# Performance work log

Measured on AMD Instinct MI355X. Metric: run time of the kernel, lower is better.

## Reference

```python
import jax, jax.numpy as jnp
import numpy as np

VOCAB, D, K = 100000, 300, 5

def setup_inputs() -> dict:
    key = jax.random.key(0)
    ks = jax.random.split(key, 12)
    B, BAG, L = 64, 16, 128
    token_ids = jax.random.randint(ks[0], (B * BAG, L), 0, VOCAB)
    mention_rep = jax.random.normal(ks[1], (B, BAG, D), dtype=jnp.float32)
    s = 0.05
    emb = jax.random.normal(ks[2], (VOCAB, D), dtype=jnp.float32)
    W1 = jax.random.normal(ks[3], (D, D), dtype=jnp.float32) * s
    b1 = jnp.zeros((D,), jnp.float32)
    conv_w = jax.random.normal(ks[4], (D, D, K), dtype=jnp.float32) * s  # [out, in, k]
    conv_b = jnp.zeros((D,), jnp.float32)
    W2 = jax.random.normal(ks[5], (2 * D, D), dtype=jnp.float32) * s
    b2 = jnp.zeros((D,), jnp.float32)
    W3 = jax.random.normal(ks[6], (D, D), dtype=jnp.float32) * s
    b3 = jnp.zeros((D,), jnp.float32)
    return {"token_ids": token_ids, "mention_rep": mention_rep, "emb": emb,
            "W1": W1, "b1": b1, "conv_w": conv_w, "conv_b": conv_b,
            "W2": W2, "b2": b2, "W3": W3, "b3": b3}

def reference(token_ids, mention_rep, emb, W1, b1, conv_w, conv_b, W2, b2, W3, b3):
    # fused gather+pad: [N, L, D]
    x = emb[token_ids]
    # lin1
    x = x @ W1 + b1
    # conv1d over time, VALID, stride 1: NCH layout
    xc = jnp.transpose(x, (0, 2, 1))  # [N, D, L]
    y = jax.lax.conv_general_dilated(xc, conv_w, (1,), 'VALID',
                                     dimension_numbers=('NCH', 'OIH', 'NCH'))
    y = y + conv_b[None, :, None]
    cnn_out = jnp.max(y, axis=-1)  # [N, D]
    m = mention_rep.reshape(mention_rep.shape[0] * mention_rep.shape[1], -1)  # dropout = identity (eval)
    concat = jnp.concatenate([cnn_out, m], axis=-1)
    h = jnp.tanh(concat @ W2 + b2)
    out = h @ W3 + b3  # dropout = identity (eval)
    return out
```

## Files before the change

kernel.cpp:

```cpp
#include <hip/hip_runtime.h>


#define DD   300
#define LL   128
#define TOUT 124
#define CH   16
#define XR   20
#define NSTG 8
#define BLK  320
#define KS     19
#define SLABP  6080
#define ROWP   20
#define WS_G1_OFF  0
#define WS_CV_OFF  194560
#define WS_NEEDED  1167360

typedef __attribute__((ext_vector_type(8))) _Float16 f16x8;
typedef __attribute__((ext_vector_type(4))) _Float16 f16x4;
typedef __attribute__((ext_vector_type(4))) float f32x4;
typedef __attribute__((ext_vector_type(16))) float f32x16;
typedef unsigned int   u32;
typedef unsigned short u16;
typedef __attribute__((ext_vector_type(4))) u32 u32x4;

__device__ __forceinline__ float b2f(u16 u) {
    union { float f; u32 i; } x; x.i = ((u32)u) << 16; return x.f;
}
__device__ __forceinline__ u16 f2bu(float f) {
    union { float f; u32 i; } x; x.f = f;
    u32 r = x.i + 0x7FFFu + ((x.i >> 16) & 1u);
    return (u16)(r >> 16);
}
__device__ __forceinline__ float ld(const void* p, size_t idx, int is32) {
    return is32 ? ((const float*)p)[idx] : b2f(((const u16*)p)[idx]);
}
__device__ __forceinline__ int sniff_is32(const void* W1) {
    int cnt = 0;
    const u32* w1raw = (const u32*)W1;
    for (int i = 0; i < 64; ++i) {
        u32 e = (w1raw[i] >> 7) & 0xFFu;
        cnt += (e >= 100u && e <= 126u) ? 1 : 0;
    }
    return (cnt < 32) ? 1 : 0;
}

__device__ __forceinline__ void barrier_lgkm() {
    asm volatile("s_waitcnt lgkmcnt(0)" ::: "memory");
    __builtin_amdgcn_s_barrier();
}
__device__ __forceinline__ void barrier_only() {
    __builtin_amdgcn_s_barrier();
}

__device__ __forceinline__ void unit_decomp(int u, int& o, int& kq) {
    kq = (u >= 912) ? 3 : (u >= 608) ? 2 : (u >= 304) ? 1 : 0;
    o  = u - 304 * kq;
}
__device__ __forceinline__ void g1_load(const float* W1f, int kk, int o, int kq, float r[4]) {
    const int kbase = kk * 16 + kq * 4;
    #pragma unroll
    for (int j = 0; j < 4; ++j) {
        const int k = kbase + j;
        r[j] = (k < DD && o < DD) ? W1f[(size_t)k * DD + o] : 0.f;
    }
}
__device__ __forceinline__ void g1_write(_Float16* Ws, int o, int kq, const float r[4]) {
    f16x4 v;
    #pragma unroll
    for (int j = 0; j < 4; ++j) v[j] = (_Float16)r[j];
    *(f16x4*)&Ws[o * ROWP + (kq << 2)] = v;
}
__device__ __forceinline__ void cv_load(const float* CWf, int kk, int o, int kq, float r[20]) {
    const int kbase = kk * 16 + kq * 4;
    const bool ok = (o < DD) && (kbase < DD);
    const float4* src = (const float4*)(CWf + (size_t)o * 1500 + kk * 80 + kq * 20);
    #pragma unroll
    for (int i = 0; i < 5; ++i) {
        float4 t = ok ? src[i] : float4{0.f, 0.f, 0.f, 0.f};
        r[4*i] = t.x; r[4*i+1] = t.y; r[4*i+2] = t.z; r[4*i+3] = t.w;
    }
}
__device__ __forceinline__ void cv_write(_Float16* Ws, int o, int kq, const float r[20]) {
    #pragma unroll
    for (int s = 0; s < 5; ++s) {
        f16x4 v;
        #pragma unroll
        for (int j = 0; j < 4; ++j) v[j] = (_Float16)r[j * 5 + s];
        *(f16x4*)&Ws[s * SLABP + o * ROWP + (kq << 2)] = v;
    }
}

__global__ void CNNEncoder_36258113912977_xform(
    const void* W1, const void* conv_w, void* ws)
{
    if (!sniff_is32(W1)) return;
    const int kk = blockIdx.x, part = blockIdx.y, tid = threadIdx.x;

    if (part == 0) {
        const float* W1f = (const float*)W1;
        f16x8* dst = (f16x8*)((char*)ws + WS_G1_OFF) + (size_t)kk * 640;
        for (int g = tid; g < 640; g += 512) {
            const int kc = (g >= 320) ? 1 : 0;
            const int nn = g - kc * 320;
            f16x8 v;
            #pragma unroll
            for (int e = 0; e < 8; ++e) {
                const int k = kk * 16 + kc * 8 + e;
                v[e] = (_Float16)((k < DD && nn < DD) ? W1f[(size_t)k * DD + nn] : 0.f);
            }
            dst[g] = v;
        }
    } else {
        const int s = part - 1;
        const float* CWf = (const float*)conv_w;
        f16x8* dst = (f16x8*)((char*)ws + WS_CV_OFF) + (size_t)kk * 3200 + (size_t)s * 640;
        for (int g = tid; g < 640; g += 512) {
            const int kc = (g >= 320) ? 1 : 0;
            const int nn = g - kc * 320;
            f16x8 v;
            #pragma unroll
            for (int e = 0; e < 8; ++e) {
                const int k = kk * 16 + kc * 8 + e;
                v[e] = (_Float16)((k < DD && nn < DD)
                        ? CWf[(size_t)nn * 1500 + (size_t)k * 5 + s] : 0.f);
            }
            dst[g] = v;
        }
    }
}

__global__ __launch_bounds__(512, 2) void CNNEncoder_36258113912977_kernel(
    const int* __restrict__ tok, const void* mention, const void* emb,
    const void* W1, const void* b1, const void* conv_w, const void* conv_b,
    const void* W2, const void* b2, const void* W3, const void* b3,
    void* out, const void* ws)
{
    if (!sniff_is32(W1)) return;

    __shared__ __align__(16) _Float16 XB[132 * 320];
    __shared__ __align__(16) _Float16 Ws[25600];
    __shared__ float pmax4[4][320];
    __shared__ float cbuf[2 * DD];
    __shared__ float hbuf[DD];

    const int n = blockIdx.x, tid = threadIdx.x;
    const int w   = tid >> 6;
    const int l   = tid & 63;
    const int l31 = l & 31, lh = l >> 5;
    const int wm  = w >> 1;
    const int wn  = w & 1;
    const int nbase = wn * 160;
    const int mrow0 = wm * 32;
    const int* trow = tok + (size_t)n * LL;

    const f16x8* wsG1 = (const f16x8*)((const char*)ws + WS_G1_OFF);
    const f16x8* wsCV = (const f16x8*)((const char*)ws + WS_CV_OFF);
    f16x8* WsV = (f16x8*)Ws;
    const bool hx = (tid < 128);

    for (int i = tid; i < 132 * 160; i += 512) ((u32*)XB)[i] = 0u;
    __syncthreads();

    {
        const int r = tid >> 2, q = tid & 3;
        const float* erow = (const float*)emb + (size_t)trow[r] * DD;
        for (int c = q; c < 38; c += 4) {
            f16x8 v;
            if (c < 37) {
                const float4 f0 = *(const float4*)(erow + 8 * c);
                const float4 f1 = *(const float4*)(erow + 8 * c + 4);
                v[0]=(_Float16)f0.x; v[1]=(_Float16)f0.y;
                v[2]=(_Float16)f0.z; v[3]=(_Float16)f0.w;
                v[4]=(_Float16)f1.x; v[5]=(_Float16)f1.y;
                v[6]=(_Float16)f1.z; v[7]=(_Float16)f1.w;
            } else {
                const float4 f0 = *(const float4*)(erow + 296);
                v[0]=(_Float16)f0.x; v[1]=(_Float16)f0.y;
                v[2]=(_Float16)f0.z; v[3]=(_Float16)f0.w;
                v[4]=(_Float16)0.f; v[5]=(_Float16)0.f;
                v[6]=(_Float16)0.f; v[7]=(_Float16)0.f;
            }
            const int p = c ^ (r & 7);
            *(f16x8*)&XB[r * 320 + (p << 3)] = v;
        }
    }

    f32x16 acc[5];
    #pragma unroll
    for (int nt = 0; nt < 5; ++nt)
        #pragma unroll
        for (int j = 0; j < 16; ++j) acc[nt][j] = 0.f;

    f16x8 sa, sb;
    f16x8 cs[7];

    sa = wsG1[tid];
    if (hx) sb = wsG1[512 + tid];
    __syncthreads();

    for (int kk = 0; kk < 19; ++kk) {
        WsV[tid] = sa;
        if (hx) WsV[512 + tid] = sb;
        barrier_lgkm();
        if (kk + 1 < 19) {
            const f16x8* src = wsG1 + (size_t)(kk + 1) * 640;
            sa = src[tid];
            if (hx) sb = src[512 + tid];
        } else {
            #pragma unroll
            for (int p = 0; p < 6; ++p) cs[p] = wsCV[tid + 512 * p];
            if (hx) cs[6] = wsCV[3072 + tid];
        }
        {
            const int c = 2 * kk + lh;
            const int row = mrow0 + l31;
            const f16x8 a = *(const f16x8*)&XB[row * 320 + ((c ^ (row & 7)) << 3)];
            __builtin_amdgcn_s_setprio(1);
            #pragma unroll
            for (int nt = 0; nt < 5; ++nt) {
                const int nn = nbase + nt * 32 + l31;
                const f16x8 b = *(const f16x8*)&Ws[lh * 2560 + nn * 8];
                acc[nt] = __builtin_amdgcn_mfma_f32_32x32x16_f16(a, b, acc[nt], 0, 0, 0);
            }
            __builtin_amdgcn_s_setprio(0);
        }
        barrier_only();
    }

    {
        const float* b1f = (const float*)b1;
        #pragma unroll
        for (int nt = 0; nt < 5; ++nt) {
            const int col = nbase + nt * 32 + l31;
            const float bb = (col < DD) ? b1f[col] : 0.f;
            const int cc = col >> 3, c7 = col & 7;
            #pragma unroll
            for (int q = 0; q < 4; ++q) {
                #pragma unroll
                for (int r = 0; r < 4; ++r) {
                    const int row = mrow0 + q * 8 + 4 * lh + r;
                    XB[row * 320 + ((cc ^ (row & 7)) << 3) + c7]
                        = (_Float16)(acc[nt][4 * q + r] + bb);
                }
            }
        }
    }

    #pragma unroll
    for (int nt = 0; nt < 5; ++nt)
        #pragma unroll
        for (int j = 0; j < 16; ++j) acc[nt][j] = 0.f;

    for (int kk = 0; kk < 19; ++kk) {
        #pragma unroll
        for (int p = 0; p < 6; ++p) WsV[tid + 512 * p] = cs[p];
        if (hx) WsV[3072 + tid] = cs[6];
        barrier_lgkm();
        if (kk + 1 < 19) {
            const f16x8* src = wsCV + (size_t)(kk + 1) * 3200;
            #pragma unroll
            for (int p = 0; p < 6; ++p) cs[p] = src[tid + 512 * p];
            if (hx) cs[6] = src[3072 + tid];
        }
        #pragma unroll
        for (int s = 0; s < 5; ++s) {
            const int c = 2 * kk + lh;
            const int row = mrow0 + l31 + s;
            const f16x8 a = *(const f16x8*)&XB[row * 320 + ((c ^ (row & 7)) << 3)];
            __builtin_amdgcn_s_setprio(1);
            #pragma unroll
            for (int nt = 0; nt < 5; ++nt) {
                const int nn = nbase + nt * 32 + l31;
                const f16x8 b = *(const f16x8*)&Ws[s * 5120 + lh * 2560 + nn * 8];
                acc[nt] = __builtin_amdgcn_mfma_f32_32x32x16_f16(a, b, acc[nt], 0, 0, 0);
            }
            __builtin_amdgcn_s_setprio(0);
        }
        barrier_only();
    }

    #pragma unroll
    for (int nt = 0; nt < 5; ++nt) {
        float m = -3.0e38f;
        #pragma unroll
        for (int q = 0; q < 4; ++q) {
            if (!(wm == 3 && q == 3)) {
                #pragma unroll
                for (int r = 0; r < 4; ++r) m = fmaxf(m, acc[nt][4 * q + r]);
            } else if (lh == 0) {
                #pragma unroll
                for (int r = 0; r < 4; ++r) m = fmaxf(m, acc[nt][12 + r]);
            }
        }
        m = fmaxf(m, __shfl_xor(m, 32));
        if (lh == 0) pmax4[wm][nbase + nt * 32 + l31] = m;
    }
    __syncthreads();

    if (tid < DD) {
        float m = fmaxf(fmaxf(pmax4[0][tid], pmax4[1][tid]),
                        fmaxf(pmax4[2][tid], pmax4[3][tid]));
        cbuf[tid]      = m + ((const float*)conv_b)[tid];
        cbuf[DD + tid] = ((const float*)mention)[(size_t)n * DD + tid];
    }
    __syncthreads();

    if (tid < DD) {
        const float* W2f = (const float*)W2;
        float a0 = 0.f, a1 = 0.f, a2 = 0.f, a3 = 0.f;
        for (int c = 0; c < 2 * DD; c += 4) {
            a0 += cbuf[c]     * W2f[(size_t)c * DD + tid];
            a1 += cbuf[c + 1] * W2f[(size_t)(c + 1) * DD + tid];
            a2 += cbuf[c + 2] * W2f[(size_t)(c + 2) * DD + tid];
            a3 += cbuf[c + 3] * W2f[(size_t)(c + 3) * DD + tid];
        }
        hbuf[tid] = tanhf(((const float*)b2)[tid] + (a0 + a1) + (a2 + a3));
    }
    __syncthreads();

    if (tid < DD) {
        const float* W3f = (const float*)W3;
        float a0 = 0.f, a1 = 0.f;
        for (int c = 0; c < DD; c += 2) {
            a0 += hbuf[c]     * W3f[(size_t)c * DD + tid];
            a1 += hbuf[c + 1] * W3f[(size_t)(c + 1) * DD + tid];
        }
        ((float*)out)[(size_t)n * DD + tid] = ((const float*)b3)[tid] + a0 + a1;
    }
}

__global__ __launch_bounds__(512, 2) void CNNEncoder_36258113912977_nows(
    const int* __restrict__ tok, const void* mention, const void* emb,
    const void* W1, const void* b1, const void* conv_w, const void* conv_b,
    const void* W2, const void* b2, const void* W3, const void* b3,
    void* out)
{
    if (!sniff_is32(W1)) return;

    __shared__ __align__(16) _Float16 XB[132 * 320];
    __shared__ __align__(16) _Float16 Ws[5 * SLABP];
    __shared__ float pmax2[2][304];
    __shared__ float cbuf[2 * DD];
    __shared__ float hbuf[DD];

    const int n = blockIdx.x, tid = threadIdx.x;
    const int w   = tid >> 6;
    const int l   = tid & 63;
    const int l15 = l & 15, lg = l >> 4;
    const int wm  = w >> 2;
    const int wn  = w & 3;
    const int ntw   = (wn < 3) ? 5 : 4;
    const int nbase = wn * 80;
    const int mrow0 = wm * 64;
    const int* trow = tok + (size_t)n * LL;
    const float* W1f = (const float*)W1;
    const float* CWf = (const float*)conv_w;

    int o0, kq0, o1, kq1, o2, kq2;
    unit_decomp(tid, o0, kq0);
    unit_decomp(512 + tid, o1, kq1);
    const bool act2 = (l < 24);
    unit_decomp(1024 + w * 24 + (l < 24 ? l : 0), o2, kq2);

    for (int i = tid; i < 132 * 160; i += 512) ((u32*)XB)[i] = 0u;
    __syncthreads();

    {
        const int r = tid >> 2, q = tid & 3;
        const float* erow = (const float*)emb + (size_t)trow[r] * DD;
        for (int c = q; c < 38; c += 4) {
            f16x8 v;
            if (c < 37) {
                const float4 f0 = *(const float4*)(erow + 8 * c);
                const float4 f1 = *(const float4*)(erow + 8 * c + 4);
                v[0]=(_Float16)f0.x; v[1]=(_Float16)f0.y;
                v[2]=(_Float16)f0.z; v[3]=(_Float16)f0.w;
                v[4]=(_Float16)f1.x; v[5]=(_Float16)f1.y;
                v[6]=(_Float16)f1.z; v[7]=(_Float16)f1.w;
            } else {
                const float4 f0 = *(const float4*)(erow + 296);
                v[0]=(_Float16)f0.x; v[1]=(_Float16)f0.y;
                v[2]=(_Float16)f0.z; v[3]=(_Float16)f0.w;
                v[4]=(_Float16)0.f; v[5]=(_Float16)0.f;
                v[6]=(_Float16)0.f; v[7]=(_Float16)0.f;
            }
            const int p = c ^ (r & 7);
            *(f16x8*)&XB[r * 320 + (p << 3)] = v;
        }
    }

    f32x4 acc[4][5];
    const f32x4 vzero = {0.f, 0.f, 0.f, 0.f};
    #pragma unroll
    for (int mt = 0; mt < 4; ++mt)
        #pragma unroll
        for (int nt = 0; nt < 5; ++nt) acc[mt][nt] = vzero;

    float g1a[4], g1b[4], g1c[4];
    float cfa[20], cfb[20], cfc[20];

    g1_load(W1f, 0, o0, kq0, g1a);
    g1_load(W1f, 0, o1, kq1, g1b);
    if (act2) g1_load(W1f, 0, o2, kq2, g1c);
    __syncthreads();

    for (int kk = 0; kk < KS; ++kk) {
        g1_write(Ws, o0, kq0, g1a);
        g1_write(Ws, o1, kq1, g1b);
        if (act2) g1_write(Ws, o2, kq2, g1c);
        barrier_lgkm();
        if (kk + 1 < KS) {
            g1_load(W1f, kk + 1, o0, kq0, g1a);
            g1_load(W1f, kk + 1, o1, kq1, g1b);
            if (act2) g1_load(W1f, kk + 1, o2, kq2, g1c);
        } else {
            cv_load(CWf, 0, o0, kq0, cfa);
            cv_load(CWf, 0, o1, kq1, cfb);
            if (act2) cv_load(CWf, 0, o2, kq2, cfc);
        }
        {
            f16x4 af[4];
            #pragma unroll
            for (int mt = 0; mt < 4; ++mt) {
                const int row = mrow0 + mt * 16 + l15;
                const int c = (kk << 1) + (lg >> 1);
                af[mt] = *(const f16x4*)&XB[row * 320 + ((c ^ (row & 7)) << 3) + ((lg & 1) << 2)];
            }
            #pragma unroll
            for (int nt = 0; nt < 5; ++nt) {
                if (nt < ntw) {
                    const int nn = nbase + nt * 16 + l15;
                    const f16x4 b = *(const f16x4*)&Ws[nn * ROWP + (lg << 2)];
                    #pragma unroll
                    for (int mt = 0; mt < 4; ++mt)
                        acc[mt][nt] = __builtin_amdgcn_mfma_f32_16x16x16f16(af[mt], b, acc[mt][nt], 0, 0, 0);
                }
            }
        }
        barrier_only();
    }

    {
        const float* b1f = (const float*)b1;
        #pragma unroll
        for (int nt = 0; nt < 5; ++nt) {
            if (nt < ntw) {
                const int col = nbase + nt * 16 + l15;
                const float bb = (col < DD) ? b1f[col] : 0.f;
                #pragma unroll
                for (int mt = 0; mt < 4; ++mt) {
                    #pragma unroll
                    for (int j = 0; j < 4; ++j) {
                        const int row = mrow0 + mt * 16 + (lg << 2) + j;
                        XB[row * 320 + (((col >> 3) ^ (row & 7)) << 3) + (col & 7)]
                            = (_Float16)(acc[mt][nt][j] + bb);
                    }
                }
            }
        }
    }

    #pragma unroll
    for (int mt = 0; mt < 4; ++mt)
        #pragma unroll
        for (int nt = 0; nt < 5; ++nt) acc[mt][nt] = vzero;

    for (int kk = 0; kk < KS; ++kk) {
        cv_write(Ws, o0, kq0, cfa);
        cv_write(Ws, o1, kq1, cfb);
        if (act2) cv_write(Ws, o2, kq2, cfc);
        barrier_lgkm();
        if (kk + 1 < KS) {
            cv_load(CWf, kk + 1, o0, kq0, cfa);
            cv_load(CWf, kk + 1, o1, kq1, cfb);
            if (act2) cv_load(CWf, kk + 1, o2, kq2, cfc);
        }
        #pragma unroll
        for (int s = 0; s < 5; ++s) {
            f16x4 af[4];
            #pragma unroll
            for (int mt = 0; mt < 4; ++mt) {
                const int row = mrow0 + mt * 16 + l15 + s;
                const int c = (kk << 1) + (lg >> 1);
                af[mt] = *(const f16x4*)&XB[row * 320 + ((c ^ (row & 7)) << 3) + ((lg & 1) << 2)];
            }
            #pragma unroll
            for (int nt = 0; nt < 5; ++nt) {
                if (nt < ntw) {
                    const int nn = nbase + nt * 16 + l15;
                    const f16x4 b = *(const f16x4*)&Ws[s * SLABP + nn * ROWP + (lg << 2)];
                    #pragma unroll
                    for (int mt = 0; mt < 4; ++mt)
                        acc[mt][nt] = __builtin_amdgcn_mfma_f32_16x16x16f16(af[mt], b, acc[mt][nt], 0, 0, 0);
                }
            }
        }
        barrier_only();
    }

    #pragma unroll
    for (int nt = 0; nt < 5; ++nt) {
        if (nt < ntw) {
            float m = -3.0e38f;
            #pragma unroll
            for (int mt = 0; mt < 4; ++mt) {
                #pragma unroll
                for (int j = 0; j < 4; ++j) {
                    const int t = mrow0 + mt * 16 + (lg << 2) + j;
                    if (t < TOUT) m = fmaxf(m, acc[mt][nt][j]);
                }
            }
            m = fmaxf(m, __shfl_xor(m, 16));
            m = fmaxf(m, __shfl_xor(m, 32));
            if (lg == 0) pmax2[wm][nbase + nt * 16 + l15] = m;
        }
    }
    __syncthreads();

    if (tid < DD) {
        const float m = fmaxf(pmax2[0][tid], pmax2[1][tid]);
        cbuf[tid]      = m + ((const float*)conv_b)[tid];
        cbuf[DD + tid] = ((const float*)mention)[(size_t)n * DD + tid];
    }
    __syncthreads();

    if (tid < DD) {
        const float* W2f = (const float*)W2;
        float a0 = 0.f, a1 = 0.f, a2 = 0.f, a3 = 0.f;
        for (int c = 0; c < 2 * DD; c += 4) {
            a0 += cbuf[c]     * W2f[(size_t)c * DD + tid];
            a1 += cbuf[c + 1] * W2f[(size_t)(c + 1) * DD + tid];
            a2 += cbuf[c + 2] * W2f[(size_t)(c + 2) * DD + tid];
            a3 += cbuf[c + 3] * W2f[(size_t)(c + 3) * DD + tid];
        }
        hbuf[tid] = tanhf(((const float*)b2)[tid] + (a0 + a1) + (a2 + a3));
    }
    __syncthreads();

    if (tid < DD) {
        const float* W3f = (const float*)W3;
        float a0 = 0.f, a1 = 0.f;
        for (int c = 0; c < DD; c += 2) {
            a0 += hbuf[c]     * W3f[(size_t)c * DD + tid];
            a1 += hbuf[c + 1] * W3f[(size_t)(c + 1) * DD + tid];
        }
        ((float*)out)[(size_t)n * DD + tid] = ((const float*)b3)[tid] + a0 + a1;
    }
}

__global__ void CNNEncoder_36258113912977_fallback(
    const int* tok, const void* mention, const void* emb,
    const void* W1, const void* b1, const void* conv_w, const void* conv_b,
    const void* W2, const void* b2, const void* W3, const void* b3,
    void* out)
{
    __shared__ float g[XR * DD];
    __shared__ float xh[XR * DD];
    __shared__ float concat[2 * DD];
    __shared__ float hbuf[DD];

    const int n = blockIdx.x, tid = threadIdx.x;
    const int* trow = tok + (size_t)n * LL;

    if (sniff_is32(W1)) return;
    const int is32 = 0;

    float mmax = -3.0e38f;

    for (int stage = 0; stage < NSTG; ++stage) {
        const int tbase = stage * CH;
        __syncthreads();

        for (int i = tid; i < XR * DD; i += BLK) {
            int r = i / DD, c = i - (i / DD) * DD;
            int gr = tbase + r; if (gr > 127) gr = 127;
            g[i] = ld(emb, (size_t)trow[gr] * DD + c, is32);
        }
        __syncthreads();

        if (tid < DD) {
            float acc[XR];
            #pragma unroll
            for (int r = 0; r < XR; ++r) acc[r] = 0.f;
            for (int k = 0; k < DD; ++k) {
                float wv = ld(W1, (size_t)k * DD + tid, is32);
                #pragma unroll
                for (int r = 0; r < XR; ++r) acc[r] += g[r * DD + k] * wv;
            }
            float bb = ld(b1, tid, is32);
            #pragma unroll
            for (int r = 0; r < XR; ++r) xh[r * DD + tid] = acc[r] + bb;
        }
        __syncthreads();

        if (tid < DD) {
            float y[CH];
            #pragma unroll
            for (int t = 0; t < CH; ++t) y[t] = 0.f;
            const size_t cwoff = (size_t)tid * (DD * 5);
            for (int k = 0; k < DD; ++k) {
                #pragma unroll
                for (int s = 0; s < 5; ++s) {
                    float wv = ld(conv_w, cwoff + k * 5 + s, is32);
                    #pragma unroll
                    for (int t = 0; t < CH; ++t)
                        y[t] += xh[(t + s) * DD + k] * wv;
                }
            }
            #pragma unroll
            for (int t = 0; t < CH; ++t) {
                int tt = tbase + t;
                if (tt < TOUT) mmax = fmaxf(mmax, y[t]);
            }
        }
    }

    __syncthreads();
    if (tid < DD) {
        concat[tid]      = mmax + ld(conv_b, tid, is32);
        concat[DD + tid] = ld(mention, (size_t)n * DD + tid, is32);
    }
    __syncthreads();

    if (tid < DD) {
        float a = ld(b2, tid, is32);
        for (int c = 0; c < 2 * DD; ++c)
            a += concat[c] * ld(W2, (size_t)c * DD + tid, is32);
        hbuf[tid] = tanhf(a);
    }
    __syncthreads();

    if (tid < DD) {
        float a = ld(b3, tid, is32);
        for (int c = 0; c < DD; ++c)
            a += hbuf[c] * ld(W3, (size_t)c * DD + tid, is32);
        ((u16*)out)[(size_t)n * DD + tid] = f2bu(a);
    }
}

extern "C" void kernel_launch(void* const* d_in, const int* in_sizes, int n_in,
                              void* d_out, int out_size, void* d_ws, size_t ws_size,
                              hipStream_t stream)
{
    if (ws_size >= (size_t)WS_NEEDED && d_ws != nullptr) {
        CNNEncoder_36258113912977_xform<<<dim3(19, 6), 512, 0, stream>>>(
            d_in[3], d_in[5], d_ws);
        CNNEncoder_36258113912977_kernel<<<1024, 512, 0, stream>>>(
            (const int*)d_in[0], d_in[1], d_in[2], d_in[3], d_in[4], d_in[5],
            d_in[6], d_in[7], d_in[8], d_in[9], d_in[10], d_out, d_ws);
    } else {
        CNNEncoder_36258113912977_nows<<<1024, 512, 0, stream>>>(
            (const int*)d_in[0], d_in[1], d_in[2], d_in[3], d_in[4], d_in[5],
            d_in[6], d_in[7], d_in[8], d_in[9], d_in[10], d_out);
    }
    CNNEncoder_36258113912977_fallback<<<1024, BLK, 0, stream>>>(
        (const int*)d_in[0], d_in[1], d_in[2], d_in[3], d_in[4], d_in[5],
        d_in[6], d_in[7], d_in[8], d_in[9], d_in[10], d_out);
}
```

Measured before the change: 462.3 us.

## Stream lin1 and conv weights through a unified 6-slot LDS ring pipeline

```diff
diff --git a/kernel.cpp b/kernel.cpp
--- a/kernel.cpp
+++ b/kernel.cpp
@@ -14,6 +14,7 @@
 #define WS_G1_OFF  0
 #define WS_CV_OFF  194560
 #define WS_NEEDED  1167360
+#define NPH        114
 
 typedef __attribute__((ext_vector_type(8))) _Float16 f16x8;
 typedef __attribute__((ext_vector_type(4))) _Float16 f16x4;
@@ -46,9 +47,6 @@
 
 __device__ __forceinline__ void barrier_lgkm() {
     asm volatile("s_waitcnt lgkmcnt(0)" ::: "memory");
-    __builtin_amdgcn_s_barrier();
-}
-__device__ __forceinline__ void barrier_only() {
     __builtin_amdgcn_s_barrier();
 }
 
@@ -129,6 +127,41 @@
     }
 }
 
+#define STAGE_PH(P, Q, QX) do {                                             \
+    const int wr_ = (P) + 5;                                                \
+    if (wr_ < NPH) {                                                        \
+        _Float16* d_ = &ring[(wr_ % 6) * 5120];                             \
+        *(u32x4*)&d_[tid * 8] = Q;                                          \
+        if (tid < 128) *(u32x4*)&d_[(512 + tid) * 8] = QX;                  \
+    }                                                                       \
+    const int lp_ = (P) + 7;                                                \
+    if (lp_ < NPH) {                                                        \
+        const u32x4* s_ = (const u32x4*)wsAll + (size_t)lp_ * 640;          \
+        Q = s_[tid];                                                        \
+        if (tid < 128) QX = s_[512 + tid];                                  \
+    }                                                                       \
+} while (0)
+
+#define PH_BODY(P, SROW, KKC, Q, QX) do {                                   \
+    STAGE_PH((P), Q, QX);                                                   \
+    const int phys_ = (P) % 6;                                              \
+    const int c_ = 2 * (KKC) + lh;                                          \
+    const int row_ = mrow0 + l31 + (SROW);                                  \
+    const f16x8 a_ = *(const f16x8*)&XB[row_ * 320 + ((c_ ^ (row_ & 7)) << 3)]; \
+    __builtin_amdgcn_s_setprio(1);                                          \
+    _Pragma("unroll")                                                       \
+    for (int nt_ = 0; nt_ < 5; ++nt_) {                                     \
+        const int nn_ = nbase + nt_ * 32 + l31;                             \
+        const f16x8 b_ = *(const f16x8*)&ring[phys_ * 5120 + lh * 2560 + nn_ * 8]; \
+        acc[nt_] = __builtin_amdgcn_mfma_f32_32x32x16_f16(a_, b_, acc[nt_], 0, 0, 0); \
+    }                                                                       \
+    __builtin_amdgcn_s_setprio(0);                                          \
+    barrier_lgkm();                                                         \
+} while (0)
+
+#define PH_G1(KK, Q, QX)    PH_BODY((KK), 0, (KK), Q, QX)
+#define PH_CV(KK, S, Q, QX) PH_BODY(19 + (KK) * 5 + (S), (S), (KK), Q, QX)
+
 __global__ __launch_bounds__(512, 2) void CNNEncoder_36258113912977_kernel(
     const int* __restrict__ tok, const void* mention, const void* emb,
     const void* W1, const void* b1, const void* conv_w, const void* conv_b,
@@ -138,7 +171,7 @@
     if (!sniff_is32(W1)) return;
 
     __shared__ __align__(16) _Float16 XB[132 * 320];
-    __shared__ __align__(16) _Float16 Ws[25600];
+    __shared__ __align__(16) _Float16 ring[6 * 5120];
     __shared__ float pmax4[4][320];
     __shared__ float cbuf[2 * DD];
     __shared__ float hbuf[DD];
@@ -152,11 +185,21 @@
     const int nbase = wn * 160;
     const int mrow0 = wm * 32;
     const int* trow = tok + (size_t)n * LL;
-
-    const f16x8* wsG1 = (const f16x8*)((const char*)ws + WS_G1_OFF);
-    const f16x8* wsCV = (const f16x8*)((const char*)ws + WS_CV_OFF);
-    f16x8* WsV = (f16x8*)Ws;
-    const bool hx = (tid < 128);
+    const void* wsAll = ws;
+
+    u32x4 qE, qO, qEx, qOx;
+    u32x4 pre[5], prex[5];
+
+    #pragma unroll
+    for (int pl = 0; pl < 5; ++pl) {
+        const u32x4* s_ = (const u32x4*)wsAll + (size_t)pl * 640;
+        pre[pl] = s_[tid];
+        if (tid < 128) prex[pl] = s_[512 + tid];
+    }
+    { const u32x4* s_ = (const u32x4*)wsAll + (size_t)5 * 640;
+      qE = s_[tid]; if (tid < 128) qEx = s_[512 + tid]; }
+    { const u32x4* s_ = (const u32x4*)wsAll + (size_t)6 * 640;
+      qO = s_[tid]; if (tid < 128) qOx = s_[512 + tid]; }
 
     for (int i = tid; i < 132 * 160; i += 512) ((u32*)XB)[i] = 0u;
     __syncthreads();
@@ -185,47 +228,24 @@
         }
     }
 
+    #pragma unroll
+    for (int pl = 0; pl < 5; ++pl) {
+        *(u32x4*)&ring[pl * 5120 + tid * 8] = pre[pl];
+        if (tid < 128) *(u32x4*)&ring[pl * 5120 + (512 + tid) * 8] = prex[pl];
+    }
+    __syncthreads();
+
     f32x16 acc[5];
     #pragma unroll
     for (int nt = 0; nt < 5; ++nt)
         #pragma unroll
         for (int j = 0; j < 16; ++j) acc[nt][j] = 0.f;
 
-    f16x8 sa, sb;
-    f16x8 cs[7];
-
-    sa = wsG1[tid];
-    if (hx) sb = wsG1[512 + tid];
-    __syncthreads();
-
-    for (int kk = 0; kk < 19; ++kk) {
-        WsV[tid] = sa;
-        if (hx) WsV[512 + tid] = sb;
-        barrier_lgkm();
-        if (kk + 1 < 19) {
-            const f16x8* src = wsG1 + (size_t)(kk + 1) * 640;
-            sa = src[tid];
-            if (hx) sb = src[512 + tid];
-        } else {
-            #pragma unroll
-            for (int p = 0; p < 6; ++p) cs[p] = wsCV[tid + 512 * p];
-            if (hx) cs[6] = wsCV[3072 + tid];
-        }
-        {
-            const int c = 2 * kk + lh;
-            const int row = mrow0 + l31;
-            const f16x8 a = *(const f16x8*)&XB[row * 320 + ((c ^ (row & 7)) << 3)];
-            __builtin_amdgcn_s_setprio(1);
-            #pragma unroll
-            for (int nt = 0; nt < 5; ++nt) {
-                const int nn = nbase + nt * 32 + l31;
-                const f16x8 b = *(const f16x8*)&Ws[lh * 2560 + nn * 8];
-                acc[nt] = __builtin_amdgcn_mfma_f32_32x32x16_f16(a, b, acc[nt], 0, 0, 0);
-            }
-            __builtin_amdgcn_s_setprio(0);
-        }
-        barrier_only();
-    }
+    for (int kk = 0; kk < 18; kk += 2) {
+        PH_G1(kk,     qE, qEx);
+        PH_G1(kk + 1, qO, qOx);
+    }
+    PH_G1(18, qE, qEx);
 
     {
         const float* b1f = (const float*)b1;
@@ -245,39 +265,24 @@
             }
         }
     }
+    __syncthreads();
 
     #pragma unroll
     for (int nt = 0; nt < 5; ++nt)
         #pragma unroll
         for (int j = 0; j < 16; ++j) acc[nt][j] = 0.f;
 
-    for (int kk = 0; kk < 19; ++kk) {
-        #pragma unroll
-        for (int p = 0; p < 6; ++p) WsV[tid + 512 * p] = cs[p];
-        if (hx) WsV[3072 + tid] = cs[6];
-        barrier_lgkm();
-        if (kk + 1 < 19) {
-            const f16x8* src = wsCV + (size_t)(kk + 1) * 3200;
-            #pragma unroll
-            for (int p = 0; p < 6; ++p) cs[p] = src[tid + 512 * p];
-            if (hx) cs[6] = src[3072 + tid];
-        }
-        #pragma unroll
-        for (int s = 0; s < 5; ++s) {
-            const int c = 2 * kk + lh;
-            const int row = mrow0 + l31 + s;
-            const f16x8 a = *(const f16x8*)&XB[row * 320 + ((c ^ (row & 7)) << 3)];
-            __builtin_amdgcn_s_setprio(1);
-            #pragma unroll
-            for (int nt = 0; nt < 5; ++nt) {
-                const int nn = nbase + nt * 32 + l31;
-                const f16x8 b = *(const f16x8*)&Ws[s * 5120 + lh * 2560 + nn * 8];
-                acc[nt] = __builtin_amdgcn_mfma_f32_32x32x16_f16(a, b, acc[nt], 0, 0, 0);
-            }
-            __builtin_amdgcn_s_setprio(0);
-        }
-        barrier_only();
-    }
+    for (int kk = 0; kk < 18; kk += 2) {
+        PH_CV(kk, 0, qO, qOx);  PH_CV(kk, 1, qE, qEx);
+        PH_CV(kk, 2, qO, qOx);  PH_CV(kk, 3, qE, qEx);
+        PH_CV(kk, 4, qO, qOx);
+        PH_CV(kk + 1, 0, qE, qEx);  PH_CV(kk + 1, 1, qO, qOx);
+        PH_CV(kk + 1, 2, qE, qEx);  PH_CV(kk + 1, 3, qO, qOx);
+        PH_CV(kk + 1, 4, qE, qEx);
+    }
+    PH_CV(18, 0, qO, qOx);  PH_CV(18, 1, qE, qEx);
+    PH_CV(18, 2, qO, qOx);  PH_CV(18, 3, qE, qEx);
+    PH_CV(18, 4, qO, qOx);
 
     #pragma unroll
     for (int nt = 0; nt < 5; ++nt) {
@@ -437,7 +442,7 @@
                 }
             }
         }
-        barrier_only();
+        __builtin_amdgcn_s_barrier();
     }
 
     {
@@ -495,7 +500,7 @@
                 }
             }
         }
-        barrier_only();
+        __builtin_amdgcn_s_barrier();
     }
 
     #pragma unroll
```

After: 466.7 us. Within noise of the previous version (+0.9%).
